# Kernel tuning notes

Measured on AMD Instinct MI355X. Metric: run time of the kernel, lower is better.

The kernel has to match this reference:

```python
import jax, jax.numpy as jnp
import numpy as np

DIM = 32
DN = ('NCDHW', 'OIDHW', 'NCDHW')


def _dwconv(x, w, b, pad, dil):
    # depthwise 3D conv, x: [N, C, D, H, W], w: [C, 1, kd, kh, kw]
    y = jax.lax.conv_general_dilated(
        x, w, window_strides=(1, 1, 1),
        padding=[(pad[0], pad[0]), (pad[1], pad[1]), (pad[2], pad[2])],
        rhs_dilation=dil, dimension_numbers=DN,
        feature_group_count=x.shape[1])
    return y + b[None, :, None, None, None]


def setup_inputs() -> dict:
    key = jax.random.key(0)
    ks = jax.random.split(key, 11)
    B, T, C, D, H, W = 1, 8, DIM, 32, 64, 64
    x = jax.random.normal(ks[0], (B, T, C, D, H, W), dtype=jnp.float32)
    s = 0.1
    w0z = jax.random.normal(ks[1], (C, 1, 3, 1, 1), dtype=jnp.float32) * s
    b0z = jax.random.normal(ks[2], (C,), dtype=jnp.float32) * s
    w0x = jax.random.normal(ks[3], (C, 1, 1, 3, 1), dtype=jnp.float32) * s
    b0x = jax.random.normal(ks[4], (C,), dtype=jnp.float32) * s
    w0y = jax.random.normal(ks[5], (C, 1, 1, 1, 3), dtype=jnp.float32) * s
    b0y = jax.random.normal(ks[6], (C,), dtype=jnp.float32) * s
    wsz = jax.random.normal(ks[7], (C, 1, 5, 1, 1), dtype=jnp.float32) * s
    bsz = jax.random.normal(ks[8], (C,), dtype=jnp.float32) * s
    wp = jax.random.normal(ks[9], (C, C, 1, 1, 1), dtype=jnp.float32) * s
    bp = jax.random.normal(ks[10], (C,), dtype=jnp.float32) * s
    return {"x": x, "w0z": w0z, "b0z": b0z, "w0x": w0x, "b0x": b0x,
            "w0y": w0y, "b0y": b0y, "wsz": wsz, "bsz": bsz,
            "wp": wp, "bp": bp}


def reference(x, w0z, b0z, w0x, b0x, w0y, b0y, wsz, bsz, wp, bp):
    B, T, C, D, H, W = x.shape
    h = x.reshape(B * T, C, D, H, W)  # TimeDistributed flatten
    res = h
    h = _dwconv(h, w0z, b0z, (1, 0, 0), (1, 1, 1))
    h = _dwconv(h, w0x, b0x, (0, 1, 0), (1, 1, 1))
    h = _dwconv(h, w0y, b0y, (0, 0, 1), (1, 1, 1))
    # forward applies conv_spatial_z three times (faithful to source)
    for _ in range(3):
        h = _dwconv(h, wsz, bsz, (4, 0, 0), (2, 1, 1))
    # pointwise 1x1x1 conv (full channel mixing)
    h = jax.lax.conv_general_dilated(
        h, wp, window_strides=(1, 1, 1),
        padding=[(0, 0)] * 3, dimension_numbers=DN)
    h = h + bp[None, :, None, None, None]
    out = res * h
    return out.reshape(B, T, C, D, H, W)
```

## Files before the change

kernel.cpp:

```cpp
#include <hip/hip_runtime.h>

constexpr int NT = 8;
constexpr int C  = 32;
constexpr int D  = 32;
constexpr int H  = 64;
constexpr int W  = 64;
constexpr int ROWS = 4;
constexpr int SP = D * H * W;
constexpr int HW = H * W;

__global__ __launch_bounds__(256, 4)
void dw_chain(const float* __restrict__ x,
              const float* __restrict__ w0z, const float* __restrict__ b0z,
              const float* __restrict__ w0x, const float* __restrict__ b0x,
              const float* __restrict__ w0y, const float* __restrict__ b0y,
              const float* __restrict__ wsz, const float* __restrict__ bsz,
              float* __restrict__ hdw)
{
    const int rr  = blockIdx.x;
    const int lid = (rr & 7) * (NT * C * (H / ROWS) / 8) + (rr >> 3);
    const int htile = lid % (H / ROWS);
    const int c     = (lid / (H / ROWS)) % C;
    const int n     = lid / ((H / ROWS) * C);

    const int tid = threadIdx.x;
    const int w   = tid & 63;
    const int hg  = __builtin_amdgcn_readfirstlane(htile * ROWS + (tid >> 6));

    const float* xc = x + ((size_t)n * C + c) * SP;

    const float wz0 = w0z[c*3+0], wz1 = w0z[c*3+1], wz2 = w0z[c*3+2];
    const float wx1 = w0x[c*3+1];
    const float wy0 = w0y[c*3+0], wy1 = w0y[c*3+1], wy2 = w0y[c*3+2];
    const float bz = b0z[c], bx = b0x[c], by = b0y[c], bs = bsz[c];
    float wsk[5];
    #pragma unroll
    for (int k = 0; k < 5; ++k) wsk[k] = wsz[c*5+k];

    const float wxk0 = (hg > 0)     ? w0x[c*3+0] : 0.f;
    const float wxk2 = (hg < H - 1) ? w0x[c*3+2] : 0.f;
    const int   hm = (hg > 0)     ? hg - 1 : 0;
    const int   hp = (hg < H - 1) ? hg + 1 : H - 1;

    const float* p0 = xc + (size_t)hm * W;
    const float* p1 = xc + (size_t)hg * W;
    const float* p2 = xc + (size_t)hp * W;

    float a0[D], a1[D], a2[D];
    #pragma unroll
    for (int d = 0; d < D; ++d) {
        a0[d] = p0[(size_t)d * HW + w];
        a1[d] = p1[(size_t)d * HW + w];
        a2[d] = p2[(size_t)d * HW + w];
    }
    #pragma unroll
    for (int d = 0; d < D; ++d)
        asm volatile("" : "+v"(a0[d]), "+v"(a1[d]), "+v"(a2[d]));

    float hrow[D];
    #pragma unroll
    for (int d = 0; d < D; ++d)
        hrow[d] = wxk0 * a0[d] + wx1 * a1[d] + wxk2 * a2[d];

    const float cb = bx + (wxk0 + wx1 + wxk2) * bz;
    float acc2[D];
    #pragma unroll
    for (int d = 0; d < D; ++d) {
        float t = cb + wz1 * hrow[d];
        if (d > 0)     t += wz0 * hrow[d - 1];
        if (d < D - 1) t += wz2 * hrow[d + 1];
        acc2[d] = t;
    }

    const bool has_l = (w > 0), has_r = (w < W - 1);
    float acc3[D];
    #pragma unroll
    for (int d = 0; d < D; ++d) {
        float left  = __shfl_up(acc2[d], 1);
        float right = __shfl_down(acc2[d], 1);
        float t = by + wy1 * acc2[d];
        if (has_l) t += wy0 * left;
        if (has_r) t += wy2 * right;
        acc3[d] = t;
    }

    #pragma unroll
    for (int it = 0; it < 3; ++it) {
        float s[D];
        #pragma unroll
        for (int d = 0; d < D; ++d) {
            float t = bs;
            #pragma unroll
            for (int k = 0; k < 5; ++k) {
                int j = d + 2 * k - 4;
                if (j >= 0 && j < D) t += wsk[k] * acc3[j];
            }
            s[d] = t;
        }
        #pragma unroll
        for (int d = 0; d < D; ++d) acc3[d] = s[d];
    }

    float* oc = hdw + ((size_t)n * C + c) * SP + (size_t)hg * W;
    #pragma unroll
    for (int d = 0; d < D; ++d) oc[(size_t)d * HW + w] = acc3[d];
}

__global__ __launch_bounds__(256)
void pw_mul(const float* __restrict__ x,
            const float* __restrict__ wp, const float* __restrict__ bp,
            float* __restrict__ io)
{
    const size_t p = (size_t)blockIdx.x * 256 + threadIdx.x;
    const size_t n  = p / SP;
    const size_t sp = p % SP;
    const size_t base = n * (size_t)C * SP + sp;

    float v[C];
    #pragma unroll
    for (int ci = 0; ci < C; ++ci) v[ci] = io[base + (size_t)ci * SP];

    for (int co = 0; co < C; ++co) {
        float y = bp[co];
        #pragma unroll
        for (int ci = 0; ci < C; ++ci) y += wp[co * C + ci] * v[ci];
        const size_t idx = base + (size_t)co * SP;
        io[idx] = x[idx] * y;
    }
}

extern "C" void kernel_launch(void* const* d_in, const int* in_sizes, int n_in,
                              void* d_out, int out_size, void* d_ws, size_t ws_size,
                              hipStream_t stream)
{
    const float* x   = (const float*)d_in[0];
    const float* w0z = (const float*)d_in[1];
    const float* b0z = (const float*)d_in[2];
    const float* w0x = (const float*)d_in[3];
    const float* b0x = (const float*)d_in[4];
    const float* w0y = (const float*)d_in[5];
    const float* b0y = (const float*)d_in[6];
    const float* wsz = (const float*)d_in[7];
    const float* bsz = (const float*)d_in[8];
    const float* wp  = (const float*)d_in[9];
    const float* bp  = (const float*)d_in[10];
    float* out = (float*)d_out;

    const int gridA = NT * C * (H / ROWS);
    dw_chain<<<gridA, 256, 0, stream>>>(x, w0z, b0z, w0x, b0x, w0y, b0y,
                                        wsz, bsz, out);

    const int positions = NT * SP;
    pw_mul<<<positions / 256, 256, 0, stream>>>(x, wp, bp, out);
}
```

Measured before the change: 112.0 us.

## Stage input halo rows in LDS via direct global-to-LDS loads

The depthwise chain kernel used to have each wavefront load three neighbouring H rows straight from global memory into registers, so every row was fetched about three times across a block. It now loads the block's 6 rows (4 plus halo) × 32 depths into shared memory once with global_load_lds, then reads the three rows per depth from LDS. This cuts redundant global traffic and register pressure from the a0/a1/a2 arrays, at the cost of 48KB LDS per block, lower occupancy (launch bounds 4→3) and a full barrier before compute.

```diff
diff --git a/kernel.cpp b/kernel.cpp
--- a/kernel.cpp
+++ b/kernel.cpp
@@ -9,7 +9,12 @@
 constexpr int SP = D * H * W;
 constexpr int HW = H * W;
 
-__global__ __launch_bounds__(256, 4)
+#define GLD_TO_LDS(gp, lp)                                              \
+    __builtin_amdgcn_global_load_lds(                                   \
+        (const __attribute__((address_space(1))) void*)(gp),            \
+        (__attribute__((address_space(3))) void*)(lp), 4, 0, 0)
+
+__global__ __launch_bounds__(256, 3)
 void dw_chain(const float* __restrict__ x,
               const float* __restrict__ w0z, const float* __restrict__ b0z,
               const float* __restrict__ w0x, const float* __restrict__ b0x,
@@ -17,17 +22,32 @@
               const float* __restrict__ wsz, const float* __restrict__ bsz,
               float* __restrict__ hdw)
 {
+    __shared__ float smem[6][D][W];
+
     const int rr  = blockIdx.x;
     const int lid = (rr & 7) * (NT * C * (H / ROWS) / 8) + (rr >> 3);
     const int htile = lid % (H / ROWS);
     const int c     = (lid / (H / ROWS)) % C;
     const int n     = lid / ((H / ROWS) * C);
+    const int h0    = htile * ROWS;
 
     const int tid = threadIdx.x;
     const int w   = tid & 63;
-    const int hg  = __builtin_amdgcn_readfirstlane(htile * ROWS + (tid >> 6));
+    const int r   = tid >> 6;
+    const int hg  = h0 + r;
 
     const float* xc = x + ((size_t)n * C + c) * SP;
+
+    for (int t = r; t < 6 * D; t += 4) {
+        const int j = t >> 5;
+        const int d = t & 31;
+        int hr = h0 - 1 + j;
+        hr = (hr < 0) ? 0 : ((hr > H - 1) ? H - 1 : hr);
+        const float* gp = xc + (size_t)d * HW + (size_t)hr * W + w;
+        GLD_TO_LDS(gp, &smem[j][d][0]);
+    }
+    asm volatile("s_waitcnt vmcnt(0)" ::: "memory");
+    __syncthreads();
 
     const float wz0 = w0z[c*3+0], wz1 = w0z[c*3+1], wz2 = w0z[c*3+2];
     const float wx1 = w0x[c*3+1];
@@ -39,28 +59,15 @@
 
     const float wxk0 = (hg > 0)     ? w0x[c*3+0] : 0.f;
     const float wxk2 = (hg < H - 1) ? w0x[c*3+2] : 0.f;
-    const int   hm = (hg > 0)     ? hg - 1 : 0;
-    const int   hp = (hg < H - 1) ? hg + 1 : H - 1;
-
-    const float* p0 = xc + (size_t)hm * W;
-    const float* p1 = xc + (size_t)hg * W;
-    const float* p2 = xc + (size_t)hp * W;
-
-    float a0[D], a1[D], a2[D];
-    #pragma unroll
-    for (int d = 0; d < D; ++d) {
-        a0[d] = p0[(size_t)d * HW + w];
-        a1[d] = p1[(size_t)d * HW + w];
-        a2[d] = p2[(size_t)d * HW + w];
-    }
-    #pragma unroll
-    for (int d = 0; d < D; ++d)
-        asm volatile("" : "+v"(a0[d]), "+v"(a1[d]), "+v"(a2[d]));
 
     float hrow[D];
     #pragma unroll
-    for (int d = 0; d < D; ++d)
-        hrow[d] = wxk0 * a0[d] + wx1 * a1[d] + wxk2 * a2[d];
+    for (int d = 0; d < D; ++d) {
+        const float a0 = smem[r    ][d][w];
+        const float a1 = smem[r + 1][d][w];
+        const float a2 = smem[r + 2][d][w];
+        hrow[d] = wxk0 * a0 + wx1 * a1 + wxk2 * a2;
+    }
 
     const float cb = bx + (wxk0 + wx1 + wxk2) * bz;
     float acc2[D];
```

Result: slower. 128.5 us (+14.7%).

## Vectorize both kernels to float2 with two W-columns per thread

Applied to the files above, without the earlier changes.

Each thread in the depthwise chain kernel now handles two adjacent W columns using float2 loads and stores. Half a wavefront covers a row, so a block covers 8 H rows, which halves the grid. The W-direction conv now uses one neighbour internal to the thread plus cross-lane shuffles. The pointwise kernel likewise processes two positions per thread with float2 loads and stores, reusing each weight load for two outputs. Register pressure roughly doubles in the depthwise kernel (two 32-deep column arrays), which may reduce occupancy under the 256x4 launch bound.

```diff
diff --git a/kernel.cpp b/kernel.cpp
--- a/kernel.cpp
+++ b/kernel.cpp
@@ -5,9 +5,16 @@
 constexpr int D  = 32;
 constexpr int H  = 64;
 constexpr int W  = 64;
-constexpr int ROWS = 4;
 constexpr int SP = D * H * W;
 constexpr int HW = H * W;
+constexpr int RPB = 8;
+
+static __device__ __forceinline__ float2 ld2(const float* p) {
+    return *reinterpret_cast<const float2*>(p);
+}
+static __device__ __forceinline__ void st2(float* p, float a, float b) {
+    *reinterpret_cast<float2*>(p) = make_float2(a, b);
+}
 
 __global__ __launch_bounds__(256, 4)
 void dw_chain(const float* __restrict__ x,
@@ -18,14 +25,17 @@
               float* __restrict__ hdw)
 {
     const int rr  = blockIdx.x;
-    const int lid = (rr & 7) * (NT * C * (H / ROWS) / 8) + (rr >> 3);
-    const int htile = lid % (H / ROWS);
-    const int c     = (lid / (H / ROWS)) % C;
-    const int n     = lid / ((H / ROWS) * C);
+    const int lid = (rr & 7) * (NT * C * (H / RPB) / 8) + (rr >> 3);
+    const int htile = lid % (H / RPB);
+    const int c     = (lid / (H / RPB)) % C;
+    const int n     = lid / ((H / RPB) * C);
 
-    const int tid = threadIdx.x;
-    const int w   = tid & 63;
-    const int hg  = __builtin_amdgcn_readfirstlane(htile * ROWS + (tid >> 6));
+    const int tid  = threadIdx.x;
+    const int lane = tid & 63;
+    const int r    = tid >> 6;
+    const int rw   = lane >> 5;
+    const int i    = lane & 31;
+    const int hg   = htile * RPB + r * 2 + rw;
 
     const float* xc = x + ((size_t)n * C + c) * SP;
 
@@ -37,73 +47,71 @@
     #pragma unroll
     for (int k = 0; k < 5; ++k) wsk[k] = wsz[c*5+k];
 
-    const float wxk0 = (hg > 0)     ? w0x[c*3+0] : 0.f;
+    const float wxk0 = (hg > 0)     ? w0z[0] * 0.f + w0x[c*3+0] : 0.f;
     const float wxk2 = (hg < H - 1) ? w0x[c*3+2] : 0.f;
     const int   hm = (hg > 0)     ? hg - 1 : 0;
     const int   hp = (hg < H - 1) ? hg + 1 : H - 1;
 
-    const float* p0 = xc + (size_t)hm * W;
-    const float* p1 = xc + (size_t)hg * W;
-    const float* p2 = xc + (size_t)hp * W;
+    const float* p0 = xc + (size_t)hm * W + 2 * i;
+    const float* p1 = xc + (size_t)hg * W + 2 * i;
+    const float* p2 = xc + (size_t)hp * W + 2 * i;
 
-    float a0[D], a1[D], a2[D];
+    float h0[D], h1[D];
     #pragma unroll
     for (int d = 0; d < D; ++d) {
-        a0[d] = p0[(size_t)d * HW + w];
-        a1[d] = p1[(size_t)d * HW + w];
-        a2[d] = p2[(size_t)d * HW + w];
+        const float2 a0 = ld2(p0 + (size_t)d * HW);
+        const float2 a1 = ld2(p1 + (size_t)d * HW);
+        const float2 a2 = ld2(p2 + (size_t)d * HW);
+        h0[d] = wxk0 * a0.x + wx1 * a1.x + wxk2 * a2.x;
+        h1[d] = wxk0 * a0.y + wx1 * a1.y + wxk2 * a2.y;
     }
-    #pragma unroll
-    for (int d = 0; d < D; ++d)
-        asm volatile("" : "+v"(a0[d]), "+v"(a1[d]), "+v"(a2[d]));
-
-    float hrow[D];
-    #pragma unroll
-    for (int d = 0; d < D; ++d)
-        hrow[d] = wxk0 * a0[d] + wx1 * a1[d] + wxk2 * a2[d];
 
     const float cb = bx + (wxk0 + wx1 + wxk2) * bz;
-    float acc2[D];
+    float za[D], zb[D];
     #pragma unroll
     for (int d = 0; d < D; ++d) {
-        float t = cb + wz1 * hrow[d];
-        if (d > 0)     t += wz0 * hrow[d - 1];
-        if (d < D - 1) t += wz2 * hrow[d + 1];
-        acc2[d] = t;
+        float t0 = cb + wz1 * h0[d];
+        float t1 = cb + wz1 * h1[d];
+        if (d > 0)     { t0 += wz0 * h0[d - 1]; t1 += wz0 * h1[d - 1]; }
+        if (d < D - 1) { t0 += wz2 * h0[d + 1]; t1 += wz2 * h1[d + 1]; }
+        za[d] = t0; zb[d] = t1;
     }
 
-    const bool has_l = (w > 0), has_r = (w < W - 1);
-    float acc3[D];
+    const float wy0l = (i > 0)  ? wy0 : 0.f;
+    const float wy2r = (i < 31) ? wy2 : 0.f;
+    float ca[D], cbb[D];
     #pragma unroll
     for (int d = 0; d < D; ++d) {
-        float left  = __shfl_up(acc2[d], 1);
-        float right = __shfl_down(acc2[d], 1);
-        float t = by + wy1 * acc2[d];
-        if (has_l) t += wy0 * left;
-        if (has_r) t += wy2 * right;
-        acc3[d] = t;
+        const float left  = __shfl_up(zb[d], 1);
+        const float right = __shfl_down(za[d], 1);
+        ca[d]  = by + wy1 * za[d] + wy0l * left  + wy2 * zb[d];
+        cbb[d] = by + wy1 * zb[d] + wy0  * za[d] + wy2r * right;
     }
 
+    auto sz3 = [&](float (&a)[D]) {
+        #pragma unroll
+        for (int it = 0; it < 3; ++it) {
+            float s[D];
+            #pragma unroll
+            for (int d = 0; d < D; ++d) {
+                float t = bs;
+                #pragma unroll
+                for (int k = 0; k < 5; ++k) {
+                    int j = d + 2 * k - 4;
+                    if (j >= 0 && j < D) t += wsk[k] * a[j];
+                }
+                s[d] = t;
+            }
+            #pragma unroll
+            for (int d = 0; d < D; ++d) a[d] = s[d];
+        }
+    };
+    sz3(ca);
+    sz3(cbb);
+
+    float* oc = hdw + ((size_t)n * C + c) * SP + (size_t)hg * W + 2 * i;
     #pragma unroll
-    for (int it = 0; it < 3; ++it) {
-        float s[D];
-        #pragma unroll
-        for (int d = 0; d < D; ++d) {
-            float t = bs;
-            #pragma unroll
-            for (int k = 0; k < 5; ++k) {
-                int j = d + 2 * k - 4;
-                if (j >= 0 && j < D) t += wsk[k] * acc3[j];
-            }
-            s[d] = t;
-        }
-        #pragma unroll
-        for (int d = 0; d < D; ++d) acc3[d] = s[d];
-    }
-
-    float* oc = hdw + ((size_t)n * C + c) * SP + (size_t)hg * W;
-    #pragma unroll
-    for (int d = 0; d < D; ++d) oc[(size_t)d * HW + w] = acc3[d];
+    for (int d = 0; d < D; ++d) st2(oc + (size_t)d * HW, ca[d], cbb[d]);
 }
 
 __global__ __launch_bounds__(256)
@@ -111,21 +119,29 @@
             const float* __restrict__ wp, const float* __restrict__ bp,
             float* __restrict__ io)
 {
-    const size_t p = (size_t)blockIdx.x * 256 + threadIdx.x;
-    const size_t n  = p / SP;
-    const size_t sp = p % SP;
-    const size_t base = n * (size_t)C * SP + sp;
+    const int pid  = blockIdx.x * 256 + threadIdx.x;
+    const int n    = pid >> 16;
+    const int sp2  = pid & 65535;
+    const size_t base = (size_t)n * C * SP + 2 * (size_t)sp2;
 
-    float v[C];
+    float v0[C], v1[C];
     #pragma unroll
-    for (int ci = 0; ci < C; ++ci) v[ci] = io[base + (size_t)ci * SP];
+    for (int ci = 0; ci < C; ++ci) {
+        const float2 u = ld2(io + base + (size_t)ci * SP);
+        v0[ci] = u.x; v1[ci] = u.y;
+    }
 
     for (int co = 0; co < C; ++co) {
-        float y = bp[co];
+        float y0 = bp[co], y1 = bp[co];
         #pragma unroll
-        for (int ci = 0; ci < C; ++ci) y += wp[co * C + ci] * v[ci];
+        for (int ci = 0; ci < C; ++ci) {
+            const float wv = wp[co * C + ci];
+            y0 += wv * v0[ci];
+            y1 += wv * v1[ci];
+        }
         const size_t idx = base + (size_t)co * SP;
-        io[idx] = x[idx] * y;
+        const float2 xv = ld2(x + idx);
+        st2(io + idx, xv.x * y0, xv.y * y1);
     }
 }
 
@@ -146,10 +162,10 @@
     const float* bp  = (const float*)d_in[10];
     float* out = (float*)d_out;
 
-    const int gridA = NT * C * (H / ROWS);
+    const int gridA = NT * C * (H / RPB);
     dw_chain<<<gridA, 256, 0, stream>>>(x, w0z, b0z, w0x, b0x, w0y, b0y,
                                         wsz, bsz, out);
 
-    const int positions = NT * SP;
-    pw_mul<<<positions / 256, 256, 0, stream>>>(x, wp, bp, out);
+    const int pairs = NT * SP / 2;
+    pw_mul<<<pairs / 256, 256, 0, stream>>>(x, wp, bp, out);
 }
```

New measurement: 187.6 us. 1.67x slower.

## Store depthwise intermediate as packed bf16 pairs in workspace

Applied to the files above, without the earlier changes.

The depthwise chain kernel now writes its intermediate as bf16 values packed two depth slices per 32-bit word into the workspace instead of fp32 into the output buffer. The pointwise kernel reads these packed words, computes two depth positions per thread, and writes the final product to the output. This roughly halves intermediate write and read traffic and removes the read-modify-write on the output buffer, at the cost of bf16 rounding of the intermediate, which may affect accuracy. The load loop also drops the asm register barrier and fuses the H-direction stencil into the load loop.

```diff
diff --git a/kernel.cpp b/kernel.cpp
--- a/kernel.cpp
+++ b/kernel.cpp
@@ -9,13 +9,22 @@
 constexpr int SP = D * H * W;
 constexpr int HW = H * W;
 
+typedef unsigned int u32;
+
+static __device__ __forceinline__ u32 f2bf(float f) {
+    u32 u = __float_as_uint(f);
+    return (u + 0x7fffu + ((u >> 16) & 1u)) >> 16;
+}
+static __device__ __forceinline__ float bf_lo(u32 v) { return __uint_as_float(v << 16); }
+static __device__ __forceinline__ float bf_hi(u32 v) { return __uint_as_float(v & 0xffff0000u); }
+
 __global__ __launch_bounds__(256, 4)
 void dw_chain(const float* __restrict__ x,
               const float* __restrict__ w0z, const float* __restrict__ b0z,
               const float* __restrict__ w0x, const float* __restrict__ b0x,
               const float* __restrict__ w0y, const float* __restrict__ b0y,
               const float* __restrict__ wsz, const float* __restrict__ bsz,
-              float* __restrict__ hdw)
+              u32* __restrict__ hws)
 {
     const int rr  = blockIdx.x;
     const int lid = (rr & 7) * (NT * C * (H / ROWS) / 8) + (rr >> 3);
@@ -46,21 +55,14 @@
     const float* p1 = xc + (size_t)hg * W;
     const float* p2 = xc + (size_t)hp * W;
 
-    float a0[D], a1[D], a2[D];
+    float hrow[D];
     #pragma unroll
     for (int d = 0; d < D; ++d) {
-        a0[d] = p0[(size_t)d * HW + w];
-        a1[d] = p1[(size_t)d * HW + w];
-        a2[d] = p2[(size_t)d * HW + w];
+        const float a0 = p0[(size_t)d * HW + w];
+        const float a1 = p1[(size_t)d * HW + w];
+        const float a2 = p2[(size_t)d * HW + w];
+        hrow[d] = wxk0 * a0 + wx1 * a1 + wxk2 * a2;
     }
-    #pragma unroll
-    for (int d = 0; d < D; ++d)
-        asm volatile("" : "+v"(a0[d]), "+v"(a1[d]), "+v"(a2[d]));
-
-    float hrow[D];
-    #pragma unroll
-    for (int d = 0; d < D; ++d)
-        hrow[d] = wxk0 * a0[d] + wx1 * a1[d] + wxk2 * a2[d];
 
     const float cb = bx + (wxk0 + wx1 + wxk2) * bz;
     float acc2[D];
@@ -101,31 +103,48 @@
         for (int d = 0; d < D; ++d) acc3[d] = s[d];
     }
 
-    float* oc = hdw + ((size_t)n * C + c) * SP + (size_t)hg * W;
+    u32* hc = hws + ((size_t)(n * C + c) * (D / 2)) * HW + (size_t)hg * W;
     #pragma unroll
-    for (int d = 0; d < D; ++d) oc[(size_t)d * HW + w] = acc3[d];
+    for (int k = 0; k < D / 2; ++k)
+        hc[(size_t)k * HW + w] = f2bf(acc3[2*k]) | (f2bf(acc3[2*k+1]) << 16);
 }
 
 __global__ __launch_bounds__(256)
 void pw_mul(const float* __restrict__ x,
+            const u32* __restrict__ hws,
             const float* __restrict__ wp, const float* __restrict__ bp,
-            float* __restrict__ io)
+            float* __restrict__ out)
 {
-    const size_t p = (size_t)blockIdx.x * 256 + threadIdx.x;
-    const size_t n  = p / SP;
-    const size_t sp = p % SP;
-    const size_t base = n * (size_t)C * SP + sp;
+    const int b    = blockIdx.x;
+    const int n    = b & 7;
+    const int pid  = (b >> 3) * 256 + threadIdx.x;
+    const int dp   = pid >> 12;
+    const int sphw = pid & 4095;
 
-    float v[C];
+    const u32* hp = hws + ((size_t)(n * C) * (D / 2) + dp) * HW + sphw;
+
+    float v0[C], v1[C];
     #pragma unroll
-    for (int ci = 0; ci < C; ++ci) v[ci] = io[base + (size_t)ci * SP];
+    for (int ci = 0; ci < C; ++ci) {
+        const u32 u = hp[(size_t)ci * (D / 2) * HW];
+        v0[ci] = bf_lo(u);
+        v1[ci] = bf_hi(u);
+    }
+
+    const size_t i0base = (size_t)n * C * SP + (size_t)(2 * dp) * HW + sphw;
 
     for (int co = 0; co < C; ++co) {
-        float y = bp[co];
+        float y0 = bp[co], y1 = bp[co];
         #pragma unroll
-        for (int ci = 0; ci < C; ++ci) y += wp[co * C + ci] * v[ci];
-        const size_t idx = base + (size_t)co * SP;
-        io[idx] = x[idx] * y;
+        for (int ci = 0; ci < C; ++ci) {
+            const float wv = wp[co * C + ci];
+            y0 += wv * v0[ci];
+            y1 += wv * v1[ci];
+        }
+        const size_t ia = i0base + (size_t)co * SP;
+        const size_t ib = ia + (size_t)HW;
+        out[ia] = x[ia] * y0;
+        out[ib] = x[ib] * y1;
     }
 }
 
@@ -145,11 +164,12 @@
     const float* wp  = (const float*)d_in[9];
     const float* bp  = (const float*)d_in[10];
     float* out = (float*)d_out;
+    u32* hws = (u32*)d_ws;
 
     const int gridA = NT * C * (H / ROWS);
     dw_chain<<<gridA, 256, 0, stream>>>(x, w0z, b0z, w0x, b0x, w0y, b0y,
-                                        wsz, bsz, out);
+                                        wsz, bsz, hws);
 
-    const int positions = NT * SP;
-    pw_mul<<<positions / 256, 256, 0, stream>>>(x, wp, bp, out);
+    const int gridB = NT * (D / 2) * HW / 256;
+    pw_mul<<<gridB, 256, 0, stream>>>(x, hws, wp, bp, out);
 }
```

Result: faster. 109.4 us (-2.3%).
